# Performance work log

Hardware: AMD Instinct MI355X
Metric: run time of the kernel (lower is better)

Reference implementation:

```python
import jax, jax.numpy as jnp
import numpy as np

IN_F, OUT_F, NB = 4096, 4096, 8
BS = IN_F // NB  # 512


def setup_inputs() -> dict:
    key = jax.random.key(0)
    k1, k2, k3, k4 = jax.random.split(key, 4)
    weight = jax.random.normal(k1, (OUT_F, IN_F), dtype=jnp.float32) * 0.02
    bias = jax.random.normal(k2, (OUT_F,), dtype=jnp.float32) * 0.02
    x = jax.random.normal(k3, (4, 2048, IN_F), dtype=jnp.float32)
    R_blocks = jax.random.normal(k4, (NB, BS, BS), dtype=jnp.float32) * 0.1
    return {"weight": weight, "bias": bias, "x": x, "R_blocks": R_blocks, "layer_idx": 0}


def cayley_transform(A):
    # A: [nb, bs, bs]; Q = (I - A_skew) @ inv(I + A_skew + 1e-6 I)
    bs = A.shape[-1]
    I = jnp.eye(bs, dtype=A.dtype)
    A_skew = 0.5 * (A - jnp.swapaxes(A, -2, -1))
    return jnp.matmul(I - A_skew, jnp.linalg.inv(I + A_skew + 1e-6 * I))


def reference(weight, bias, x, R_blocks, layer_idx):
    R_ortho = cayley_transform(R_blocks)  # [nb, bs, bs]
    # weight @ block_diag(R) == per-block contraction on the in_features axis
    w = weight.reshape(OUT_F, NB, BS)
    tw = jnp.einsum('onb,nbc->onc', w, R_ortho).reshape(OUT_F, IN_F)
    # F.linear: x @ tw.T + bias
    out = jnp.einsum('bsi,oi->bso', x, tw) + bias
    return out
```

## Files before the change

### kernel.cpp

```cpp
#include <hip/hip_runtime.h>
#include <hip/hip_bf16.h>


typedef unsigned short u16;
typedef __attribute__((ext_vector_type(8))) __bf16 bf16x8;
typedef __attribute__((ext_vector_type(4))) float f32x4;
typedef __attribute__((ext_vector_type(8))) unsigned short u16x8;
typedef __attribute__((ext_vector_type(4))) unsigned short u16x4;

#define C0   1.000001f
#define C1Q  2.000001f
#define AS1 __attribute__((address_space(1)))
#define AS3 __attribute__((address_space(3)))

__device__ __forceinline__ u16 f2bf(float x) {
  union { float f; unsigned u; } v; v.f = x;
  return (u16)((v.u + 0x7fffu + ((v.u >> 16) & 1u)) >> 16);
}
__device__ __forceinline__ float bf2f(u16 h) {
  union { float f; unsigned u; } v; v.u = ((unsigned)h) << 16; return v.f;
}

__global__ __launch_bounds__(256) void k_build_M(const float* __restrict__ R,
                                                 u16* __restrict__ Mh,
                                                 u16* __restrict__ Ml) {
  __shared__ float t1[32][33];
  const int n = blockIdx.z;
  const int tr = blockIdx.y * 32, tc = blockIdx.x * 32;
  const int ly = threadIdx.x >> 5, lx = threadIdx.x & 31;
  const float* Rb = R + (size_t)n * 262144;
  float a[4];
#pragma unroll
  for (int i = 0; i < 4; ++i) {
    a[i] = Rb[(size_t)(tr + ly + i * 8) * 512 + tc + lx];
    t1[ly + i * 8][lx] = Rb[(size_t)(tc + ly + i * 8) * 512 + tr + lx];
  }
  __syncthreads();
#pragma unroll
  for (int i = 0; i < 4; ++i) {
    const int r = tr + ly + i * 8, c = tc + lx;
    float m = 0.5f * (a[i] - t1[lx][ly + i * 8]) + (r == c ? C0 : 0.0f);
    u16 h = f2bf(m);
    const size_t idx = (size_t)n * 262144 + (size_t)r * 512 + c;
    Mh[idx] = h;
    Ml[idx] = f2bf(m - bf2f(h));
  }
}

__global__ __launch_bounds__(1024) void k_frob_alpha(const u16* __restrict__ G2,
                                                     float* __restrict__ coef) {
  __shared__ float red[16];
  const int n = blockIdx.x, tid = threadIdx.x;
  const u16* src = G2 + (size_t)n * 262144;
  float s = 0.f;
  for (int i = tid; i < 32768; i += 1024) {
    u16x8 v = reinterpret_cast<const u16x8*>(src)[i];
#pragma unroll
    for (int e = 0; e < 8; ++e) { float f = bf2f(v[e]); s += f * f; }
  }
  for (int off = 32; off; off >>= 1) s += __shfl_down(s, off, 64);
  if ((tid & 63) == 0) red[tid >> 6] = s;
  __syncthreads();
  if (tid == 0) {
    float t = 0.f;
    for (int q = 0; q < 16; ++q) t += red[q];
    float lam = powf(t, 0.25f);
    float a = 2.0f / (C0 * C0 + lam);
    coef[n] = a;
    float e = (lam - C0 * C0) / (lam + C0 * C0);
    float sq = e * e;
    float c1 = 2.0f / (2.0f - sq);
    coef[8 + n]  = 2.0f * c1;
    coef[16 + n] = -c1 * a;
    coef[24 + n] = 2.0f * c1 * a;
    coef[32 + n] = -c1 * a * a;
    e = sq / (2.0f - sq);
    sq = e * e;
    float c2 = 2.0f / (2.0f - sq);
    coef[40 + n] = 2.0f * c2;
    coef[48 + n] = -c2;
    e = sq / (2.0f - sq);
    sq = e * e;
    float c3 = 2.0f / (2.0f - sq);
    coef[56 + n] = 2.0f * c3;
    coef[64 + n] = -c3;
  }
}

__global__ __launch_bounds__(256) void k_init(const u16* __restrict__ Mh,
                                              const u16* __restrict__ Ml,
                                              const u16* __restrict__ G,
                                              const u16* __restrict__ G2,
                                              const float* __restrict__ coef,
                                              u16* __restrict__ X0,
                                              u16* __restrict__ T2) {
  int idx = blockIdx.x * 256 + threadIdx.x;
  int n = idx >> 18, r = (idx >> 9) & 511, c = idx & 511;
  float m = bf2f(Mh[idx]) + bf2f(Ml[idx]);
  X0[idx] = f2bf(coef[n] * ((r == c ? 2.0f * C0 : 0.0f) - m));
  T2[idx] = f2bf(coef[24 + n] * bf2f(G[idx]) + coef[32 + n] * bf2f(G2[idx]));
}

#define BMM_FRAGS(rs)                                                          \
  bf16x8 a[2], b[2], al2[2], bl2[2];                                           \
  _Pragma("unroll")                                                            \
  for (int i = 0; i < 2; ++i) {                                                \
    const int fr = wr * 32 + i * 16 + c15;                                     \
    const int ia = (rs) * 2048 + fr * 32 + ((lk ^ (fr & 3)) * 8);              \
    a[i] = *reinterpret_cast<const bf16x8*>(&sA[ia]);                          \
    if constexpr (PROD3) al2[i] = *reinterpret_cast<const bf16x8*>(&sAl[ia]);  \
  }                                                                            \
  _Pragma("unroll")                                                            \
  for (int j = 0; j < 2; ++j) {                                                \
    const int fc = wc * 32 + j * 16 + c15;                                     \
    const int ib = (rs) * 2048 + fc * 32 + ((lk ^ (fc & 3)) * 8);              \
    b[j] = *reinterpret_cast<const bf16x8*>(&sB[ib]);                          \
    if constexpr (PROD3) bl2[j] = *reinterpret_cast<const bf16x8*>(&sBl[ib]);  \
  }                                                                            \
  _Pragma("unroll")                                                            \
  for (int i = 0; i < 2; ++i)                                                  \
    _Pragma("unroll")                                                          \
    for (int j = 0; j < 2; ++j) {                                              \
      acc[i][j] = __builtin_amdgcn_mfma_f32_16x16x32_bf16(a[i], b[j], acc[i][j], 0, 0, 0); \
      if constexpr (PROD3) {                                                   \
        acc[i][j] = __builtin_amdgcn_mfma_f32_16x16x32_bf16(a[i],   bl2[j], acc[i][j], 0, 0, 0); \
        acc[i][j] = __builtin_amdgcn_mfma_f32_16x16x32_bf16(al2[i], b[j],   acc[i][j], 0, 0, 0); \
      }                                                                        \
    }

#define BMM_WAIT(SEL)                                                          \
  if ((SEL) == 0) {                                                            \
    if constexpr (PROD3) asm volatile("s_waitcnt vmcnt(8)" ::: "memory");      \
    else                 asm volatile("s_waitcnt vmcnt(4)" ::: "memory");      \
  } else if ((SEL) == 1) {                                                     \
    if constexpr (PROD3) asm volatile("s_waitcnt vmcnt(4)" ::: "memory");      \
    else                 asm volatile("s_waitcnt vmcnt(2)" ::: "memory");      \
  } else {                                                                     \
    asm volatile("s_waitcnt vmcnt(0)" ::: "memory");                           \
  }

template <int PROD3, int DMODE, int OMODE, int DUAL>
__global__ __launch_bounds__(256)
void k_bmm(const u16* __restrict__ Ah, const u16* __restrict__ Al,
           const u16* __restrict__ Bh, const u16* __restrict__ Bl,
           const u16* __restrict__ Dh, const u16* __restrict__ Dl,
           u16* __restrict__ Cnh, u16* __restrict__ Cnl,
           u16* __restrict__ Cth, u16* __restrict__ Ctl,
           float cd, float cs,
           const float* __restrict__ cdp, const float* __restrict__ csp,
           const float* __restrict__ cvsrc, u16* __restrict__ cvdst, int zmm,
           const u16* __restrict__ A2, const u16* __restrict__ B2,
           const u16* __restrict__ D2, u16* __restrict__ C2) {
  __shared__ __align__(16) u16 sA[4 * 2048], sB[4 * 2048];
  __shared__ __align__(16) u16 sAl[PROD3 ? 4 * 2048 : 8];
  __shared__ __align__(16) u16 sBl[PROD3 ? 4 * 2048 : 8];

  if ((int)blockIdx.z >= zmm) {
    const int zi = ((int)blockIdx.z - zmm) * 64 + blockIdx.y * 8 + blockIdx.x;
    const int chunk = zi >> 7;
    const int base = (zi & 127) * 256 + (int)threadIdx.x;
    const float* src = cvsrc + (size_t)chunk * 4194304;
    u16* dst = cvdst + (size_t)chunk * 4194304;
#pragma unroll
    for (int e = 0; e < 16; ++e) {
      const size_t g = (size_t)(base + e * 32768) * 8;
      float4 f0 = *reinterpret_cast<const float4*>(src + g);
      float4 f1 = *reinterpret_cast<const float4*>(src + g + 4);
      u16x8 w;
      w[0] = f2bf(f0.x); w[1] = f2bf(f0.y); w[2] = f2bf(f0.z); w[3] = f2bf(f0.w);
      w[4] = f2bf(f1.x); w[5] = f2bf(f1.y); w[6] = f2bf(f1.z); w[7] = f2bf(f1.w);
      *reinterpret_cast<u16x8*>(dst + g) = w;
    }
    return;
  }

  const int zq = DUAL ? ((blockIdx.z >> 3) & 1) : 0;
  const u16* Ah_ = (DUAL && zq) ? A2 : Ah;
  const u16* Bh_ = (DUAL && zq) ? B2 : Bh;
  const u16* Dh_ = (DUAL && zq) ? D2 : Dh;
  u16* Cnh_ = (DUAL && zq) ? C2 : Cnh;
  const size_t zb = (size_t)(blockIdx.z & 7) * 262144;
  const int tid = threadIdx.x, lane = tid & 63, wave = tid >> 6;
  const int m0 = blockIdx.y * 64, n0 = blockIdx.x * 64;
  const int wr = wave >> 1, wc = wave & 1;
  const int c15 = lane & 15, lk = lane >> 4;
  const int srow = tid >> 2;
  const int sg = (tid & 3) ^ (srow & 3);
  f32x4 acc[2][2] = {};
  const u16* pa = Ah_ + zb + (size_t)(m0 + srow) * 512 + sg * 8;
  const u16* pb = Bh_ + zb + (size_t)(n0 + srow) * 512 + sg * 8;
  const u16* pal = PROD3 ? Al + zb + (size_t)(m0 + srow) * 512 + sg * 8 : pa;
  const u16* pbl = PROD3 ? Bl + zb + (size_t)(n0 + srow) * 512 + sg * 8 : pb;

  int jn = 0, js = 0;
  auto STG = [&]() {
    if (jn < 16) {
      const int off = jn << 5;
      __builtin_amdgcn_global_load_lds((const AS1 void*)(pa + off),
                                       (AS3 void*)(sA + js * 2048 + tid * 8), 16, 0, 0);
      __builtin_amdgcn_global_load_lds((const AS1 void*)(pb + off),
                                       (AS3 void*)(sB + js * 2048 + tid * 8), 16, 0, 0);
      if constexpr (PROD3) {
        __builtin_amdgcn_global_load_lds((const AS1 void*)(pal + off),
                                         (AS3 void*)(sAl + js * 2048 + tid * 8), 16, 0, 0);
        __builtin_amdgcn_global_load_lds((const AS1 void*)(pbl + off),
                                         (AS3 void*)(sBl + js * 2048 + tid * 8), 16, 0, 0);
      }
    }
    ++jn; js = (js + 1) & 3;
  };

  STG(); STG();
  int rs = 0;
  for (int t = 0; t < 14; ++t) {
    STG();
    BMM_WAIT(0)
    __builtin_amdgcn_s_barrier();
    BMM_FRAGS(rs)
    rs = (rs + 1) & 3;
  }
  STG();
  BMM_WAIT(1)
  __builtin_amdgcn_s_barrier();
  { BMM_FRAGS(rs) }
  rs = (rs + 1) & 3;
  STG();
  BMM_WAIT(2)
  __builtin_amdgcn_s_barrier();
  { BMM_FRAGS(rs) }

  const float cdL = cdp ? cdp[blockIdx.z & 7] : cd;
  const float csL = csp ? csp[blockIdx.z & 7] : cs;
#pragma unroll
  for (int i = 0; i < 2; ++i)
#pragma unroll
    for (int j = 0; j < 2; ++j) {
      const int rowb = m0 + wr * 32 + i * 16 + lk * 4;
      const int col  = n0 + wc * 32 + j * 16 + c15;
      u16 hv[4], lv[4];
#pragma unroll
      for (int r = 0; r < 4; ++r) {
        float val = csL * acc[i][j][r];
        if constexpr (DMODE >= 1) {
          float d = bf2f(Dh_[zb + (size_t)(rowb + r) * 512 + col]);
          if constexpr (DMODE == 2) d += bf2f(Dl[zb + (size_t)(rowb + r) * 512 + col]);
          val += cdL * d;
        }
        u16 h = f2bf(val);
        if constexpr (OMODE & 1) Cnh_[zb + (size_t)(rowb + r) * 512 + col] = h;
        u16 l = 0;
        if constexpr (OMODE & 10) l = f2bf(val - bf2f(h));
        if constexpr (OMODE & 2) Cnl[zb + (size_t)(rowb + r) * 512 + col] = l;
        hv[r] = h; lv[r] = l;
      }
      if constexpr (OMODE & 4) {
        u16x4 v; v[0] = hv[0]; v[1] = hv[1]; v[2] = hv[2]; v[3] = hv[3];
        *reinterpret_cast<u16x4*>(&Cth[zb + (size_t)col * 512 + rowb]) = v;
      }
      if constexpr (OMODE & 8) {
        u16x4 v; v[0] = lv[0]; v[1] = lv[1]; v[2] = lv[2]; v[3] = lv[3];
        *reinterpret_cast<u16x4*>(&Ctl[zb + (size_t)col * 512 + rowb]) = v;
      }
    }
}

__global__ __launch_bounds__(256)
void k_twmm(const u16* __restrict__ W, const u16* __restrict__ Qt,
            u16* __restrict__ tw) {
  __shared__ __align__(16) u16 sA[4 * 2048], sB[4 * 2048];
  const int z = blockIdx.z;
  const size_t zb = (size_t)z * 262144;
  const int tid = threadIdx.x, lane = tid & 63, wave = tid >> 6;
  const int m0 = blockIdx.y * 64, n0 = blockIdx.x * 64;
  const int wr = wave >> 1, wc = wave & 1;
  const int c15 = lane & 15, lk = lane >> 4;
  const int srow = tid >> 2;
  const int sg = (tid & 3) ^ (srow & 3);
  f32x4 acc[2][2] = {};
  const u16* pa = W + (size_t)(m0 + srow) * 4096 + z * 512 + sg * 8;
  const u16* pb = Qt + zb + (size_t)(n0 + srow) * 512 + sg * 8;

  int jn = 0, js = 0;
  auto STG = [&]() {
    if (jn < 16) {
      const int off = jn << 5;
      __builtin_amdgcn_global_load_lds((const AS1 void*)(pa + off),
                                       (AS3 void*)(sA + js * 2048 + tid * 8), 16, 0, 0);
      __builtin_amdgcn_global_load_lds((const AS1 void*)(pb + off),
                                       (AS3 void*)(sB + js * 2048 + tid * 8), 16, 0, 0);
    }
    ++jn; js = (js + 1) & 3;
  };

#define TW_FRAGS(rs)                                                           \
  {                                                                            \
    bf16x8 a[2], b[2];                                                         \
    _Pragma("unroll")                                                          \
    for (int i = 0; i < 2; ++i) {                                              \
      const int fr = wr * 32 + i * 16 + c15;                                   \
      a[i] = *reinterpret_cast<const bf16x8*>(                                 \
          &sA[(rs) * 2048 + fr * 32 + ((lk ^ (fr & 3)) * 8)]);                 \
    }                                                                          \
    _Pragma("unroll")                                                          \
    for (int j = 0; j < 2; ++j) {                                              \
      const int fc = wc * 32 + j * 16 + c15;                                   \
      b[j] = *reinterpret_cast<const bf16x8*>(                                 \
          &sB[(rs) * 2048 + fc * 32 + ((lk ^ (fc & 3)) * 8)]);                 \
    }                                                                          \
    _Pragma("unroll")                                                          \
    for (int i = 0; i < 2; ++i)                                                \
      _Pragma("unroll")                                                        \
      for (int j = 0; j < 2; ++j)                                              \
        acc[i][j] = __builtin_amdgcn_mfma_f32_16x16x32_bf16(a[i], b[j], acc[i][j], 0, 0, 0); \
  }

  STG(); STG();
  int rs = 0;
  for (int t = 0; t < 14; ++t) {
    STG();
    asm volatile("s_waitcnt vmcnt(4)" ::: "memory");
    __builtin_amdgcn_s_barrier();
    TW_FRAGS(rs)
    rs = (rs + 1) & 3;
  }
  STG();
  asm volatile("s_waitcnt vmcnt(2)" ::: "memory");
  __builtin_amdgcn_s_barrier();
  TW_FRAGS(rs)
  rs = (rs + 1) & 3;
  STG();
  asm volatile("s_waitcnt vmcnt(0)" ::: "memory");
  __builtin_amdgcn_s_barrier();
  TW_FRAGS(rs)

#pragma unroll
  for (int i = 0; i < 2; ++i)
#pragma unroll
    for (int j = 0; j < 2; ++j) {
      const int rowb = m0 + wr * 32 + i * 16 + lk * 4;
      const int col  = z * 512 + n0 + wc * 32 + j * 16 + c15;
#pragma unroll
      for (int r = 0; r < 4; ++r)
        tw[(size_t)(rowb + r) * 4096 + col] = f2bf(acc[i][j][r]);
    }
}

#define NSL 18

#define RD_A3(dst, MH)                                                         \
  _Pragma("unroll")                                                            \
  for (int m = 0; m < 4; ++m)                                                  \
    dst[m] = *reinterpret_cast<const bf16x8*>(                                 \
        &lds[aslot * 4096 + ((MH) * 64 + m * 16 + c15) * 32 + gsw * 8]);

#define RD_B3(dst)                                                             \
  _Pragma("unroll")                                                            \
  for (int n = 0; n < 4; ++n)                                                  \
    dst[n] = *reinterpret_cast<const bf16x8*>(                                 \
        &lds[bslot * 4096 + (bq64 + n * 16 + c15) * 32 + gsw * 8]);

#define MFMA16(afX, bfX, MH)                                                   \
  __builtin_amdgcn_s_setprio(1);                                               \
  _Pragma("unroll")                                                            \
  for (int m = 0; m < 4; ++m)                                                  \
    _Pragma("unroll")                                                          \
    for (int n = 0; n < 4; ++n)                                                \
      acc[(MH) * 4 + m][n] = __builtin_amdgcn_mfma_f32_16x16x32_bf16(          \
          afX[m], bfX[n], acc[(MH) * 4 + m][n], 0, 0, 0);                      \
  __builtin_amdgcn_s_setprio(0);

#define TILE32(WM)                                                             \
  {                                                                            \
    int aslot = s0 + wr;            if (aslot >= NSL) aslot -= NSL;            \
    int bslot = s0 + 2 + (wc >> 1); if (bslot >= NSL) bslot -= NSL;            \
    STAGE(); STAGE();                                                          \
    RD_B3(bfr)                                                                 \
    RD_A3(afA, 0)                                                              \
    MFMA16(afA, bfr, 0)                                                        \
    STAGE(); STAGE();                                                          \
    RD_A3(afB, 1)                                                              \
    MFMA16(afB, bfr, 1)                                                        \
    if ((WM) == 1) asm volatile("s_waitcnt vmcnt(8)" ::: "memory");            \
    if ((WM) == 2) asm volatile("s_waitcnt vmcnt(4)" ::: "memory");            \
    if ((WM) == 3) asm volatile("s_waitcnt vmcnt(0)" ::: "memory");            \
    if ((WM) != 0) {                                                           \
      __builtin_amdgcn_s_barrier();                                            \
      __builtin_amdgcn_sched_barrier(0);                                       \
    }                                                                          \
    s0 += 4; if (s0 >= NSL) s0 -= NSL;                                         \
  }

__global__ __launch_bounds__(512, 2)
void k_gemm256(const u16* __restrict__ A, const u16* __restrict__ B,
               const float* __restrict__ bias,
               float* __restrict__ C, int N, int K) {
  __shared__ __align__(16) u16 lds[NSL * 4096];
  const int tid = threadIdx.x, lane = tid & 63, wave = tid >> 6;
  int bid = blockIdx.y * gridDim.x + blockIdx.x;
  const int cpx = (gridDim.x * gridDim.y) >> 3;
  bid = (bid & 7) * cpx + (bid >> 3);
  const int nbx = N >> 8;
  const int bx = bid % nbx, by = bid / nbx;
  const int m0 = by << 8, n0 = bx << 8;
  const int wr = wave >> 2, wc = wave & 3;
  const int srow = tid >> 2;
  const int sgc  = (tid & 3) ^ ((srow >> 1) & 3);
  const int c15 = lane & 15, lq = lane >> 4;
  const int gsw = lq ^ ((c15 >> 1) & 3);
  const int bq64 = (wc & 1) * 64;
  const int NT = K >> 5;

  f32x4 acc[8][4] = {};
  bf16x8 afA[4], afB[4], bfr[4];

  int jn = 0, js = 0;
  auto STAGE = [&]() {
    if (jn < 4 * NT) {
      const int t = jn >> 2, q = jn & 3;
      const u16* srcb = (q < 2)
          ? A + (size_t)(m0 + q * 128 + srow) * (size_t)K
          : B + (size_t)(n0 + (q - 2) * 128 + srow) * (size_t)K;
      const u16* src = srcb + (t << 5) + sgc * 8;
      u16* dst = (u16*)lds + js * 4096 + tid * 8;
      __builtin_amdgcn_global_load_lds(
          (const AS1 void*)src, (AS3 void*)dst, 16, 0, 0);
    }
    ++jn; js = (js == NSL - 1) ? 0 : js + 1;
  };

#pragma unroll
  for (int i = 0; i < 12; ++i) STAGE();
  asm volatile("s_waitcnt vmcnt(8)" ::: "memory");
  __builtin_amdgcn_s_barrier();
  __builtin_amdgcn_sched_barrier(0);

  int s0 = 0;
  for (int tau = 0; tau < NT - 3; ++tau) {
    TILE32(1)
  }
  TILE32(2)
  TILE32(3)
  TILE32(0)

#pragma unroll
  for (int n = 0; n < 4; ++n) {
    const int col = n0 + wc * 64 + n * 16 + c15;
    const float bv = bias[col];
#pragma unroll
    for (int mi = 0; mi < 8; ++mi) {
      const int rowb = m0 + wr * 128 + mi * 16 + (lq << 2);
#pragma unroll
      for (int r = 0; r < 4; ++r)
        C[(size_t)(rowb + r) * N + col] = acc[mi][n][r] + bv;
    }
  }
}

extern "C" void kernel_launch(void* const* d_in, const int* in_sizes, int n_in,
                              void* d_out, int out_size, void* d_ws, size_t ws_size,
                              hipStream_t stream) {
  const float* W    = (const float*)d_in[0];
  const float* bias = (const float*)d_in[1];
  const float* x    = (const float*)d_in[2];
  const float* R    = (const float*)d_in[3];
  float* out = (float*)d_out;

  char* ws = (char*)d_ws;
  u16* x_bf = (u16*)(ws);
  u16* tw   = (u16*)(ws + 67108864);
  u16* W_bf = (u16*)(ws + 100663296);

  char* arena = (char*)d_out;
  auto slot = [&](int i) -> u16* { return (u16*)(arena + (size_t)i * 4194304); };
  u16 *Mh = slot(0), *Ml = slot(1);
  u16 *G = slot(2), *G2 = slot(3);
  u16 *X0 = slot(5), *T2 = slot(6), *X1 = slot(7), *X2 = slot(8), *T3 = slot(9);
  u16 *X3h = slot(10), *X3l = slot(11), *X3th = slot(12), *X3tl = slot(13);
  u16 *Tpth = slot(14), *Tptl = slot(15);
  u16 *X4h = slot(16), *X4l = slot(17), *X4th = slot(18), *X4tl = slot(19);
  u16 *Qt = slot(20);
  float* coef = (float*)(arena + (size_t)21 * 4194304);

  const u16* NUL = nullptr;
  const float* NULF = nullptr;
  u16* NULW = nullptr;
  const dim3 gC0(8, 8, 8);
  const dim3 gC2(8, 8, 12);

  k_build_M<<<dim3(16, 16, 8), 256, 0, stream>>>(R, Mh, Ml);
  k_bmm<0, 0, 1, 0><<<gC2, 256, 0, stream>>>(Mh, NUL, Mh, NUL, NUL, NUL,
      G, NULW, NULW, NULW, 0.f, 1.f, NULF, NULF, W, W_bf, 8, NUL, NUL, NUL, NULW);
  k_bmm<0, 0, 1, 0><<<gC2, 256, 0, stream>>>(G, NUL, G, NUL, NUL, NUL,
      G2, NULW, NULW, NULW, 0.f, 1.f, NULF, NULF,
      W + (size_t)2 * 4194304, W_bf + (size_t)2 * 4194304, 8, NUL, NUL, NUL, NULW);
  k_frob_alpha<<<8, 1024, 0, stream>>>(G2, coef);
  k_init<<<8192, 256, 0, stream>>>(Mh, Ml, G, G2, coef, X0, T2);
  k_bmm<0, 1, 1, 0><<<gC2, 256, 0, stream>>>(X0, NUL, G, NUL, X0, NUL,
      X1, NULW, NULW, NULW, 0.f, 0.f, coef + 8, coef + 16,
      x, x_bf, 8, NUL, NUL, NUL, NULW);
  k_bmm<0, 1, 1, 1><<<dim3(8, 8, 20), 256, 0, stream>>>(X1, NUL, T2, NUL, X1, NUL,
      X2, NULW, NULW, NULW, 0.f, 0.f, coef + 40, coef + 48,
      x + (size_t)2 * 4194304, x_bf + (size_t)2 * 4194304, 16, T2, T2, T2, T3);
  k_bmm<0, 1, 15, 0><<<gC2, 256, 0, stream>>>(X2, NUL, T3, NUL, X2, NUL,
      X3h, X3l, X3th, X3tl, 0.f, 0.f, coef + 56, coef + 64,
      x + (size_t)4 * 4194304, x_bf + (size_t)4 * 4194304, 8, NUL, NUL, NUL, NULW);
  k_bmm<1, 0, 12, 0><<<gC2, 256, 0, stream>>>(Mh, Ml, X3th, X3tl, NUL, NUL,
      NULW, NULW, Tpth, Tptl, 0.f, 1.f, NULF, NULF,
      x + (size_t)6 * 4194304, x_bf + (size_t)6 * 4194304, 8, NUL, NUL, NUL, NULW);
  k_bmm<1, 2, 15, 0><<<gC0, 256, 0, stream>>>(X3h, X3l, Tpth, Tptl, X3h, X3l,
      X4h, X4l, X4th, X4tl, 2.f, -1.f, NULF, NULF,
      x, x_bf, 8, NUL, NUL, NUL, NULW);
  k_bmm<1, 2, 4, 0><<<gC0, 256, 0, stream>>>(Mh, Ml, X4th, X4tl, X4h, X4l,
      NULW, NULW, Qt, NULW, C1Q, -1.f, NULF, NULF,
      x, x_bf, 8, NUL, NUL, NUL, NULW);
  k_twmm<<<dim3(8, 64, 8), 256, 0, stream>>>(W_bf, Qt, tw);
  k_gemm256<<<dim3(16, 32), 512, 0, stream>>>(x_bf, tw, bias, out, 4096, 4096);
}
```

Before: 502.9 us.

## Fuse Frobenius-norm reduction into G² matmul epilogue and vectorize init

```diff
diff --git a/kernel.cpp b/kernel.cpp
--- a/kernel.cpp
+++ b/kernel.cpp
@@ -19,6 +19,21 @@
 }
 __device__ __forceinline__ float bf2f(u16 h) {
   union { float f; unsigned u; } v; v.u = ((unsigned)h) << 16; return v.f;
+}
+
+__device__ __forceinline__ void get_coefs(float t, float* C) {
+  float lam = powf(t, 0.25f);
+  float a = 2.0f / (C0 * C0 + lam);
+  float e = (lam - C0 * C0) / (lam + C0 * C0);
+  float sq = e * e, c1 = 2.0f / (2.0f - sq);
+  C[0] = a; C[1] = 2.0f * c1; C[2] = -c1 * a;
+  C[3] = 2.0f * c1 * a; C[4] = -c1 * a * a;
+  e = sq / (2.0f - sq); sq = e * e;
+  float c2 = 2.0f / (2.0f - sq);
+  C[5] = 2.0f * c2; C[6] = -c2;
+  e = sq / (2.0f - sq); sq = e * e;
+  float c3 = 2.0f / (2.0f - sq);
+  C[7] = 2.0f * c3; C[8] = -c3;
 }
 
 __global__ __launch_bounds__(256) void k_build_M(const float* __restrict__ R,
@@ -47,58 +62,49 @@
   }
 }
 
-__global__ __launch_bounds__(1024) void k_frob_alpha(const u16* __restrict__ G2,
-                                                     float* __restrict__ coef) {
-  __shared__ float red[16];
-  const int n = blockIdx.x, tid = threadIdx.x;
-  const u16* src = G2 + (size_t)n * 262144;
-  float s = 0.f;
-  for (int i = tid; i < 32768; i += 1024) {
-    u16x8 v = reinterpret_cast<const u16x8*>(src)[i];
-#pragma unroll
-    for (int e = 0; e < 8; ++e) { float f = bf2f(v[e]); s += f * f; }
-  }
-  for (int off = 32; off; off >>= 1) s += __shfl_down(s, off, 64);
-  if ((tid & 63) == 0) red[tid >> 6] = s;
-  __syncthreads();
-  if (tid == 0) {
-    float t = 0.f;
-    for (int q = 0; q < 16; ++q) t += red[q];
-    float lam = powf(t, 0.25f);
-    float a = 2.0f / (C0 * C0 + lam);
-    coef[n] = a;
-    float e = (lam - C0 * C0) / (lam + C0 * C0);
-    float sq = e * e;
-    float c1 = 2.0f / (2.0f - sq);
-    coef[8 + n]  = 2.0f * c1;
-    coef[16 + n] = -c1 * a;
-    coef[24 + n] = 2.0f * c1 * a;
-    coef[32 + n] = -c1 * a * a;
-    e = sq / (2.0f - sq);
-    sq = e * e;
-    float c2 = 2.0f / (2.0f - sq);
-    coef[40 + n] = 2.0f * c2;
-    coef[48 + n] = -c2;
-    e = sq / (2.0f - sq);
-    sq = e * e;
-    float c3 = 2.0f / (2.0f - sq);
-    coef[56 + n] = 2.0f * c3;
-    coef[64 + n] = -c3;
-  }
-}
-
 __global__ __launch_bounds__(256) void k_init(const u16* __restrict__ Mh,
                                               const u16* __restrict__ Ml,
                                               const u16* __restrict__ G,
                                               const u16* __restrict__ G2,
-                                              const float* __restrict__ coef,
+                                              const float* __restrict__ part,
+                                              float* __restrict__ coef,
                                               u16* __restrict__ X0,
                                               u16* __restrict__ T2) {
-  int idx = blockIdx.x * 256 + threadIdx.x;
-  int n = idx >> 18, r = (idx >> 9) & 511, c = idx & 511;
-  float m = bf2f(Mh[idx]) + bf2f(Ml[idx]);
-  X0[idx] = f2bf(coef[n] * ((r == c ? 2.0f * C0 : 0.0f) - m));
-  T2[idx] = f2bf(coef[24 + n] * bf2f(G[idx]) + coef[32 + n] * bf2f(G2[idx]));
+  __shared__ float sp[64];
+  __shared__ float sc[9];
+  const int n = blockIdx.x >> 7;
+  if (threadIdx.x < 64) sp[threadIdx.x] = part[n * 64 + threadIdx.x];
+  __syncthreads();
+  if (threadIdx.x == 0) {
+    float s = 0.f;
+    for (int i = 0; i < 64; ++i) s += sp[i];
+    float C[9];
+    get_coefs(s, C);
+#pragma unroll
+    for (int k = 0; k < 9; ++k) sc[k] = C[k];
+    coef[n] = C[0];
+    coef[8 + n]  = C[1]; coef[16 + n] = C[2];
+    coef[24 + n] = C[3]; coef[32 + n] = C[4];
+    coef[40 + n] = C[5]; coef[48 + n] = C[6];
+    coef[56 + n] = C[7]; coef[64 + n] = C[8];
+  }
+  __syncthreads();
+  const size_t base = ((size_t)blockIdx.x * 256 + threadIdx.x) * 8;
+  const int r  = (int)((base >> 9) & 511);
+  const int c0 = (int)(base & 511);
+  u16x8 mh = *reinterpret_cast<const u16x8*>(Mh + base);
+  u16x8 ml = *reinterpret_cast<const u16x8*>(Ml + base);
+  u16x8 g  = *reinterpret_cast<const u16x8*>(G  + base);
+  u16x8 g2 = *reinterpret_cast<const u16x8*>(G2 + base);
+  u16x8 x0, t2;
+#pragma unroll
+  for (int e = 0; e < 8; ++e) {
+    float m = bf2f(mh[e]) + bf2f(ml[e]);
+    x0[e] = f2bf(sc[0] * ((r == c0 + e ? 2.0f * C0 : 0.0f) - m));
+    t2[e] = f2bf(sc[3] * bf2f(g[e]) + sc[4] * bf2f(g2[e]));
+  }
+  *reinterpret_cast<u16x8*>(X0 + base) = x0;
+  *reinterpret_cast<u16x8*>(T2 + base) = t2;
 }
 
 #define BMM_FRAGS(rs)                                                          \
@@ -139,7 +145,7 @@
     asm volatile("s_waitcnt vmcnt(0)" ::: "memory");                           \
   }
 
-template <int PROD3, int DMODE, int OMODE, int DUAL>
+template <int PROD3, int DMODE, int OMODE, int DUAL, int FROB>
 __global__ __launch_bounds__(256)
 void k_bmm(const u16* __restrict__ Ah, const u16* __restrict__ Al,
            const u16* __restrict__ Bh, const u16* __restrict__ Bl,
@@ -150,10 +156,12 @@
            const float* __restrict__ cdp, const float* __restrict__ csp,
            const float* __restrict__ cvsrc, u16* __restrict__ cvdst, int zmm,
            const u16* __restrict__ A2, const u16* __restrict__ B2,
-           const u16* __restrict__ D2, u16* __restrict__ C2) {
+           const u16* __restrict__ D2, u16* __restrict__ C2,
+           float* __restrict__ part) {
   __shared__ __align__(16) u16 sA[4 * 2048], sB[4 * 2048];
   __shared__ __align__(16) u16 sAl[PROD3 ? 4 * 2048 : 8];
   __shared__ __align__(16) u16 sBl[PROD3 ? 4 * 2048 : 8];
+  __shared__ float fred[FROB ? 4 : 1];
 
   if ((int)blockIdx.z >= zmm) {
     const int zi = ((int)blockIdx.z - zmm) * 64 + blockIdx.y * 8 + blockIdx.x;
@@ -231,6 +239,7 @@
 
   const float cdL = cdp ? cdp[blockIdx.z & 7] : cd;
   const float csL = csp ? csp[blockIdx.z & 7] : cs;
+  float fs = 0.f;
 #pragma unroll
   for (int i = 0; i < 2; ++i)
 #pragma unroll
@@ -248,6 +257,7 @@
         }
         u16 h = f2bf(val);
         if constexpr (OMODE & 1) Cnh_[zb + (size_t)(rowb + r) * 512 + col] = h;
+        if constexpr (FROB) { float v = bf2f(h); fs += v * v; }
         u16 l = 0;
         if constexpr (OMODE & 10) l = f2bf(val - bf2f(h));
         if constexpr (OMODE & 2) Cnl[zb + (size_t)(rowb + r) * 512 + col] = l;
@@ -262,6 +272,14 @@
         *reinterpret_cast<u16x4*>(&Ctl[zb + (size_t)col * 512 + rowb]) = v;
       }
     }
+  if constexpr (FROB) {
+    for (int off = 32; off; off >>= 1) fs += __shfl_down(fs, off, 64);
+    if ((tid & 63) == 0) fred[tid >> 6] = fs;
+    __syncthreads();
+    if (tid == 0)
+      part[(blockIdx.z & 7) * 64 + blockIdx.y * 8 + blockIdx.x] =
+          fred[0] + fred[1] + fred[2] + fred[3];
+  }
 }
 
 __global__ __launch_bounds__(256)
@@ -480,39 +498,45 @@
   u16 *X4h = slot(16), *X4l = slot(17), *X4th = slot(18), *X4tl = slot(19);
   u16 *Qt = slot(20);
   float* coef = (float*)(arena + (size_t)21 * 4194304);
+  float* part = coef + 1024;
 
   const u16* NUL = nullptr;
   const float* NULF = nullptr;
   u16* NULW = nullptr;
+  float* NULP = nullptr;
   const dim3 gC0(8, 8, 8);
   const dim3 gC2(8, 8, 12);
 
   k_build_M<<<dim3(16, 16, 8), 256, 0, stream>>>(R, Mh, Ml);
-  k_bmm<0, 0, 1, 0><<<gC2, 256, 0, stream>>>(Mh, NUL, Mh, NUL, NUL, NUL,
-      G, NULW, NULW, NULW, 0.f, 1.f, NULF, NULF, W, W_bf, 8, NUL, NUL, NUL, NULW);
-  k_bmm<0, 0, 1, 0><<<gC2, 256, 0, stream>>>(G, NUL, G, NUL, NUL, NUL,
+  k_bmm<0, 0, 1, 0, 0><<<gC2, 256, 0, stream>>>(Mh, NUL, Mh, NUL, NUL, NUL,
+      G, NULW, NULW, NULW, 0.f, 1.f, NULF, NULF, W, W_bf, 8,
+      NUL, NUL, NUL, NULW, NULP);
+  k_bmm<0, 0, 1, 0, 1><<<gC2, 256, 0, stream>>>(G, NUL, G, NUL, NUL, NUL,
       G2, NULW, NULW, NULW, 0.f, 1.f, NULF, NULF,
-      W + (size_t)2 * 4194304, W_bf + (size_t)2 * 4194304, 8, NUL, NUL, NUL, NULW);
-  k_frob_alpha<<<8, 1024, 0, stream>>>(G2, coef);
-  k_init<<<8192, 256, 0, stream>>>(Mh, Ml, G, G2, coef, X0, T2);
-  k_bmm<0, 1, 1, 0><<<gC2, 256, 0, stream>>>(X0, NUL, G, NUL, X0, NUL,
+      W + (size_t)2 * 4194304, W_bf + (size_t)2 * 4194304, 8,
+      NUL, NUL, NUL, NULW, part);
+  k_init<<<1024, 256, 0, stream>>>(Mh, Ml, G, G2, part, coef, X0, T2);
+  k_bmm<0, 1, 1, 0, 0><<<gC2, 256, 0, stream>>>(X0, NUL, G, NUL, X0, NUL,
       X1, NULW, NULW, NULW, 0.f, 0.f, coef + 8, coef + 16,
-      x, x_bf, 8, NUL, NUL, NUL, NULW);
-  k_bmm<0, 1, 1, 1><<<dim3(8, 8, 20), 256, 0, stream>>>(X1, NUL, T2, NUL, X1, NUL,
+      x, x_bf, 8, NUL, NUL, NUL, NULW, NULP);
+  k_bmm<0, 1, 1, 1, 0><<<dim3(8, 8, 20), 256, 0, stream>>>(X1, NUL, T2, NUL, X1, NUL,
       X2, NULW, NULW, NULW, 0.f, 0.f, coef + 40, coef + 48,
-      x + (size_t)2 * 4194304, x_bf + (size_t)2 * 4194304, 16, T2, T2, T2, T3);
-  k_bmm<0, 1, 15, 0><<<gC2, 256, 0, stream>>>(X2, NUL, T3, NUL, X2, NUL,
+      x + (size_t)2 * 4194304, x_bf + (size_t)2 * 4194304, 16,
+      T2, T2, T2, T3, NULP);
+  k_bmm<0, 1, 15, 0, 0><<<gC2, 256, 0, stream>>>(X2, NUL, T3, NUL, X2, NUL,
       X3h, X3l, X3th, X3tl, 0.f, 0.f, coef + 56, coef + 64,
-      x + (size_t)4 * 4194304, x_bf + (size_t)4 * 4194304, 8, NUL, NUL, NUL, NULW);
-  k_bmm<1, 0, 12, 0><<<gC2, 256, 0, stream>>>(Mh, Ml, X3th, X3tl, NUL, NUL,
+      x + (size_t)4 * 4194304, x_bf + (size_t)4 * 4194304, 8,
+      NUL, NUL, NUL, NULW, NULP);
+  k_bmm<1, 0, 12, 0, 0><<<gC2, 256, 0, stream>>>(Mh, Ml, X3th, X3tl, NUL, NUL,
       NULW, NULW, Tpth, Tptl, 0.f, 1.f, NULF, NULF,
-      x + (size_t)6 * 4194304, x_bf + (size_t)6 * 4194304, 8, NUL, NUL, NUL, NULW);
-  k_bmm<1, 2, 15, 0><<<gC0, 256, 0, stream>>>(X3h, X3l, Tpth, Tptl, X3h, X3l,
+      x + (size_t)6 * 4194304, x_bf + (size_t)6 * 4194304, 8,
+      NUL, NUL, NUL, NULW, NULP);
+  k_bmm<1, 2, 15, 0, 0><<<gC0, 256, 0, stream>>>(X3h, X3l, Tpth, Tptl, X3h, X3l,
       X4h, X4l, X4th, X4tl, 2.f, -1.f, NULF, NULF,
-      x, x_bf, 8, NUL, NUL, NUL, NULW);
-  k_bmm<1, 2, 4, 0><<<gC0, 256, 0, stream>>>(Mh, Ml, X4th, X4tl, X4h, X4l,
+      x, x_bf, 8, NUL, NUL, NUL, NULW, NULP);
+  k_bmm<1, 2, 4, 0, 0><<<gC0, 256, 0, stream>>>(Mh, Ml, X4th, X4tl, X4h, X4l,
       NULW, NULW, Qt, NULW, C1Q, -1.f, NULF, NULF,
-      x, x_bf, 8, NUL, NUL, NUL, NULW);
+      x, x_bf, 8, NUL, NUL, NUL, NULW, NULP);
   k_twmm<<<dim3(8, 64, 8), 256, 0, stream>>>(W_bf, Qt, tw);
   k_gemm256<<<dim3(16, 32), 512, 0, stream>>>(x_bf, tw, bias, out, 4096, 4096);
 }
```

After: 488.6 us. 2.8% less time.
